# Performance work log

Measured on AMD Instinct MI355X. Metric: run time of the kernel, lower is better.

The kernel has to match this reference:

```python
import jax, jax.numpy as jnp
import numpy as np


def setup_inputs() -> dict:
    key = jax.random.key(0)
    ks = jax.random.split(key, 8)
    B, L, d_model = 2, 4096, 1024
    d_inner, d_state, d_conv, dt_rank = 2048, 16, 4, 64
    f = jnp.float32
    g = lambda k, shape, scale: jax.random.normal(k, shape, dtype=f) * scale
    # dt bias init: inverse-softplus of dt ~ U[log 1e-3, log 1e-1] (as in Mamba)
    dt = jnp.exp(jax.random.uniform(ks[5], (d_inner,), f) * (np.log(0.1) - np.log(0.001)) + np.log(0.001))
    dt = jnp.clip(dt, 1e-4, None)
    inv_dt = dt + jnp.log(-jnp.expm1(-dt))
    A_log = jnp.log(jnp.broadcast_to(jnp.arange(1, d_state + 1, dtype=f), (d_inner, d_state)))
    return {
        "hidden_states": jax.random.normal(ks[0], (B, L, d_model), f),
        "in_proj_w": g(ks[1], (2 * d_inner, d_model), 0.02),
        "conv_w": g(ks[2], (d_inner, d_conv), 0.1),
        "conv_b": jnp.zeros((d_inner,), f),
        "x_proj_w": g(ks[3], (dt_rank + 2 * d_state, d_inner), 0.02),
        "dt_proj_w": g(ks[4], (d_inner, dt_rank), dt_rank ** -0.5),
        "dt_proj_b": inv_dt,
        "A_log": A_log,
        "D": jnp.ones((d_inner,), f),
        "out_proj_w": g(ks[6], (d_model, d_inner), 0.02),
    }


def reference(hidden_states, in_proj_w, conv_w, conv_b, x_proj_w, dt_proj_w, dt_proj_b, A_log, D, out_proj_w):
    B_, L, _ = hidden_states.shape
    d_inner, d_conv = conv_w.shape
    dt_rank = dt_proj_w.shape[1]
    d_state = A_log.shape[1]

    # input projection -> x, z gates (B, L, d_inner) each
    xz = jnp.einsum('bld,ed->ble', hidden_states, in_proj_w)
    x, z = jnp.split(xz, 2, axis=-1)

    # causal depthwise conv1d over time + SiLU
    xc = jnp.transpose(x, (0, 2, 1))                       # (B, d_inner, L)
    kern = conv_w[:, None, :]                              # (O=d_inner, I/g=1, W)
    xc = jax.lax.conv_general_dilated(
        xc, kern, window_strides=(1,), padding=[(d_conv - 1, 0)],
        dimension_numbers=('NCH', 'OIH', 'NCH'), feature_group_count=d_inner)
    xc = xc + conv_b[None, :, None]
    x = jax.nn.silu(jnp.transpose(xc, (0, 2, 1)))          # (B, L, d_inner)

    # data-dependent SSM parameters
    x_dbl = jnp.einsum('bld,kd->blk', x, x_proj_w)         # (B, L, dt_rank+2n)
    dt, Bm, Cm = jnp.split(x_dbl, [dt_rank, dt_rank + d_state], axis=-1)
    dt = jnp.einsum('blr,dr->bld', dt, dt_proj_w)
    dt = jax.nn.softplus(dt + dt_proj_b)                   # delta_softplus + delta_bias
    A = -jnp.exp(A_log)                                    # (d_inner, d_state)

    # selective scan over the sequence dim; carry h: (B, d_inner, d_state)
    def step(h, inp):
        x_t, dt_t, B_t, C_t = inp                          # (B,d) (B,d) (B,n) (B,n)
        dA = jnp.exp(dt_t[..., None] * A)                  # (B, d, n)
        h = h * dA + (dt_t * x_t)[..., None] * B_t[:, None, :]
        y = jnp.einsum('bdn,bn->bd', h, C_t)
        return h, y

    h0 = jnp.zeros((B_, d_inner, d_state), x.dtype)
    xs = (jnp.transpose(x, (1, 0, 2)), jnp.transpose(dt, (1, 0, 2)),
          jnp.transpose(Bm, (1, 0, 2)), jnp.transpose(Cm, (1, 0, 2)))
    _, ys = jax.lax.scan(step, h0, xs)                     # ys: (L, B, d_inner)

    y = jnp.transpose(ys, (1, 0, 2)) + x * D               # skip via D
    y = y * jax.nn.silu(z)                                 # gate
    return jnp.einsum('bld,od->blo', y, out_proj_w)        # (B, L, d_model)
```

## Files before the change

### kernel.cpp

```cpp
#include <hip/hip_runtime.h>
#include <cmath>

#define CH 64
#define NC 64

typedef __bf16 bf16_t;
typedef __attribute__((ext_vector_type(8))) __bf16 bf16x8;
typedef __attribute__((ext_vector_type(4))) __bf16 bf16x4;
typedef __attribute__((ext_vector_type(4))) float f32x4;

#define GLOAD_LDS16(gp, lp)                                                     \
    __builtin_amdgcn_global_load_lds(                                           \
        (const __attribute__((address_space(1))) unsigned int*)(uintptr_t)(gp), \
        (__attribute__((address_space(3))) unsigned int*)(uintptr_t)(lp),       \
        16, 0, 0)

__global__ __launch_bounds__(256) void split5n(
    const float* __restrict__ a, bf16_t* __restrict__ ah, int n4a,
    const float* __restrict__ b, bf16_t* __restrict__ bh, int n4b,
    const float* __restrict__ c, bf16_t* __restrict__ ch, bf16_t* __restrict__ cl, int n4c,
    const float* __restrict__ d, bf16_t* __restrict__ dh, bf16_t* __restrict__ dl, int n4d,
    const float* __restrict__ e, bf16_t* __restrict__ eh, int n4e)
{
    int i = blockIdx.x * 256 + threadIdx.x;
    if (i < n4a) {
        const float4 v = ((const float4*)a)[i];
        bf16x4 hv = {(bf16_t)v.x, (bf16_t)v.y, (bf16_t)v.z, (bf16_t)v.w};
        ((bf16x4*)ah)[i] = hv;
        return;
    }
    i -= n4a;
    if (i < n4b) {
        const float4 v = ((const float4*)b)[i];
        bf16x4 hv = {(bf16_t)v.x, (bf16_t)v.y, (bf16_t)v.z, (bf16_t)v.w};
        ((bf16x4*)bh)[i] = hv;
        return;
    }
    i -= n4b;
    if (i >= n4c + n4d) {
        i -= n4c + n4d;
        if (i < n4e) {
            const float4 v = ((const float4*)e)[i];
            bf16x4 hv = {(bf16_t)v.x, (bf16_t)v.y, (bf16_t)v.z, (bf16_t)v.w};
            ((bf16x4*)eh)[i] = hv;
        }
        return;
    }
    const float* src; bf16_t* hp; bf16_t* lp;
    if (i < n4c) { src = c; hp = ch; lp = cl; }
    else         { i -= n4c; src = d; hp = dh; lp = dl; }

    const float4 v = ((const float4*)src)[i];
    const bf16_t h0 = (bf16_t)v.x, h1 = (bf16_t)v.y,
                 h2 = (bf16_t)v.z, h3 = (bf16_t)v.w;
    bf16x4 hv = {h0, h1, h2, h3};
    bf16x4 lv = {(bf16_t)(v.x - (float)h0), (bf16_t)(v.y - (float)h1),
                 (bf16_t)(v.z - (float)h2), (bf16_t)(v.w - (float)h3)};
    ((bf16x4*)hp)[i] = hv;
    ((bf16x4*)lp)[i] = lv;
}

__global__ __launch_bounds__(256) void add8_split(
    const float* __restrict__ p, float* __restrict__ o,
    bf16_t* __restrict__ dth, bf16_t* __restrict__ dtl,
    int n4, size_t stride4)
{
    const int i = blockIdx.x * 256 + threadIdx.x;
    if (i >= n4) return;
    float4 s = make_float4(0.f, 0.f, 0.f, 0.f);
#pragma unroll
    for (int k = 0; k < 8; ++k) {
        const float4 v = ((const float4*)p)[(size_t)k * stride4 + i];
        s.x += v.x; s.y += v.y; s.z += v.z; s.w += v.w;
    }
    ((float4*)o)[i] = s;

    const int col4 = i % 24;
    if (col4 < 16) {
        const int row = i / 24;
        const bf16_t h0 = (bf16_t)s.x, h1 = (bf16_t)s.y,
                     h2 = (bf16_t)s.z, h3 = (bf16_t)s.w;
        bf16x4 hv = {h0, h1, h2, h3};
        bf16x4 lv = {(bf16_t)(s.x - (float)h0), (bf16_t)(s.y - (float)h1),
                     (bf16_t)(s.z - (float)h2), (bf16_t)(s.w - (float)h3)};
        ((bf16x4*)dth)[(size_t)row * 16 + col4] = hv;
        ((bf16x4*)dtl)[(size_t)row * 16 + col4] = lv;
    }
}

__global__ __launch_bounds__(256) void in_proj_fused1(
    const bf16_t* __restrict__ Ah, const bf16_t* __restrict__ Wh,
    bf16_t* __restrict__ X, bf16_t* __restrict__ Z, int Ktot)
{
    __shared__ __align__(16) bf16_t Ash[128 * 32];
    __shared__ __align__(16) bf16_t Bsh[128 * 32];

    const int tid  = threadIdx.x;
    const int lane = tid & 63;
    const int w    = tid >> 6;
    const int wr   = (w >> 1) * 64;
    const int wc   = (w & 1) * 64;
    const int bm   = blockIdx.x * 128;
    const int by   = blockIdx.y;
    const int bnW  = by * 128;
    const int l16  = lane & 15;
    const int lhi  = lane >> 4;

    f32x4 acc[4][4];
#pragma unroll
    for (int i = 0; i < 4; ++i)
#pragma unroll
        for (int j = 0; j < 4; ++j)
#pragma unroll
            for (int r = 0; r < 4; ++r) acc[i][j][r] = 0.f;

    const int srow0 = tid >> 2;
    const int sks   = (tid & 3) << 3;
    const int ldsb0 = tid * 16;

    for (int k0 = 0; k0 < Ktot; k0 += 32) {
        __syncthreads();
#pragma unroll
        for (int call = 0; call < 2; ++call) {
            const int row = srow0 + call * 64;
            const int wb  = ldsb0 + call * 4096;
            GLOAD_LDS16(Ah + (size_t)(bm + row) * Ktot + k0 + sks, (char*)Ash + wb);
            GLOAD_LDS16(Wh + (size_t)(bnW + row) * Ktot + k0 + sks, (char*)Bsh + wb);
        }
        __syncthreads();

        bf16x8 af[4], bfr[4];
#pragma unroll
        for (int f = 0; f < 4; ++f) {
            af[f]  = *(const bf16x8*)&Ash[(wr + f * 16 + l16) * 32 + lhi * 8];
            bfr[f] = *(const bf16x8*)&Bsh[(wc + f * 16 + l16) * 32 + lhi * 8];
        }
#pragma unroll
        for (int fm = 0; fm < 4; ++fm)
#pragma unroll
            for (int fn = 0; fn < 4; ++fn)
                acc[fm][fn] = __builtin_amdgcn_mfma_f32_16x16x32_bf16(
                    af[fm], bfr[fn], acc[fm][fn], 0, 0, 0);
    }

    bf16_t* outp = (by < 16) ? X : Z;
    const int bnC = ((by < 16) ? by : (by - 16)) * 128;
#pragma unroll
    for (int fm = 0; fm < 4; ++fm) {
        const int row0 = bm + wr + fm * 16 + lhi * 4;
#pragma unroll
        for (int fn = 0; fn < 4; ++fn) {
            const int col = bnC + wc + fn * 16 + l16;
#pragma unroll
            for (int r = 0; r < 4; ++r)
                outp[(size_t)(row0 + r) * 2048 + col] = (bf16_t)acc[fm][fn][r];
        }
    }
}

__global__ __launch_bounds__(256) void gemm_mfma3dt(
    const bf16_t* __restrict__ Ah, const bf16_t* __restrict__ Al,
    const bf16_t* __restrict__ Bh, const bf16_t* __restrict__ Bl,
    bf16_t* __restrict__ C, const float* __restrict__ bias,
    int Ktot, int ldc)
{
    __shared__ __align__(16) bf16_t Ash[128 * 32];
    __shared__ __align__(16) bf16_t Asl[128 * 32];
    __shared__ __align__(16) bf16_t Bsh[128 * 32];
    __shared__ __align__(16) bf16_t Bsl[128 * 32];

    const int tid  = threadIdx.x;
    const int lane = tid & 63;
    const int w    = tid >> 6;
    const int wr   = (w >> 1) * 64;
    const int wc   = (w & 1) * 64;
    const int bm   = blockIdx.x * 128;
    const int bn   = blockIdx.y * 128;
    const int l16  = lane & 15;
    const int lhi  = lane >> 4;

    f32x4 acc[4][4];
#pragma unroll
    for (int i = 0; i < 4; ++i)
#pragma unroll
        for (int j = 0; j < 4; ++j)
#pragma unroll
            for (int r = 0; r < 4; ++r) acc[i][j][r] = 0.f;

    const int srow0 = tid >> 2;
    const int sks   = (tid & 3) << 3;
    const int ldsb0 = tid * 16;

    for (int k0 = 0; k0 < Ktot; k0 += 32) {
        __syncthreads();
#pragma unroll
        for (int call = 0; call < 2; ++call) {
            const int row = srow0 + call * 64;
            const int wb  = ldsb0 + call * 4096;
            const size_t aoff = (size_t)(bm + row) * Ktot + k0 + sks;
            const size_t boff = (size_t)(bn + row) * Ktot + k0 + sks;
            GLOAD_LDS16(Ah + aoff, (char*)Ash + wb);
            GLOAD_LDS16(Al + aoff, (char*)Asl + wb);
            GLOAD_LDS16(Bh + boff, (char*)Bsh + wb);
            GLOAD_LDS16(Bl + boff, (char*)Bsl + wb);
        }
        __syncthreads();

        bf16x8 ah[4], al[4], bh[4], bl[4];
#pragma unroll
        for (int f = 0; f < 4; ++f) {
            const int ar = (wr + f * 16 + l16) * 32 + lhi * 8;
            const int br = (wc + f * 16 + l16) * 32 + lhi * 8;
            ah[f] = *(const bf16x8*)&Ash[ar];
            al[f] = *(const bf16x8*)&Asl[ar];
            bh[f] = *(const bf16x8*)&Bsh[br];
            bl[f] = *(const bf16x8*)&Bsl[br];
        }
#pragma unroll
        for (int fm = 0; fm < 4; ++fm)
#pragma unroll
            for (int fn = 0; fn < 4; ++fn) {
                acc[fm][fn] = __builtin_amdgcn_mfma_f32_16x16x32_bf16(
                    ah[fm], bh[fn], acc[fm][fn], 0, 0, 0);
                acc[fm][fn] = __builtin_amdgcn_mfma_f32_16x16x32_bf16(
                    al[fm], bh[fn], acc[fm][fn], 0, 0, 0);
                acc[fm][fn] = __builtin_amdgcn_mfma_f32_16x16x32_bf16(
                    ah[fm], bl[fn], acc[fm][fn], 0, 0, 0);
            }
    }

#pragma unroll
    for (int fm = 0; fm < 4; ++fm) {
        const int row0 = bm + wr + fm * 16 + lhi * 4;
#pragma unroll
        for (int fn = 0; fn < 4; ++fn) {
            const int col = bn + wc + fn * 16 + l16;
#pragma unroll
            for (int r = 0; r < 4; ++r) {
                float v = acc[fm][fn][r] + bias[col];
                v = (v > 20.f) ? v : log1pf(expf(v));
                C[(size_t)(row0 + r) * ldc + col] = (bf16_t)v;
            }
        }
    }
}

__global__ __launch_bounds__(256) void gemm_mfma3x(
    const bf16_t* __restrict__ Ah, const bf16_t* __restrict__ Al,
    const bf16_t* __restrict__ Bh, const bf16_t* __restrict__ Bl,
    float* __restrict__ C, int Ktot, int Ksplit, size_t partStride)
{
    __shared__ __align__(16) bf16_t Ash[128 * 32];
    __shared__ __align__(16) bf16_t Asl[128 * 32];
    __shared__ __align__(16) bf16_t Bsh[128 * 32];
    __shared__ __align__(16) bf16_t Bsl[128 * 32];

    const int tid  = threadIdx.x;
    const int lane = tid & 63;
    const int w    = tid >> 6;
    const int wr   = (w >> 1) * 64;
    const int wc   = (w & 1) * 64;
    const int bm   = blockIdx.x * 128;
    const int l16  = lane & 15;
    const int lhi  = lane >> 4;

    f32x4 acc[4][4];
#pragma unroll
    for (int i = 0; i < 4; ++i)
#pragma unroll
        for (int j = 0; j < 4; ++j)
#pragma unroll
            for (int r = 0; r < 4; ++r) acc[i][j][r] = 0.f;

    const int srow0 = tid >> 2;
    const int sks   = (tid & 3) << 3;
    const int ldsb0 = tid * 16;

    const int kBeg = blockIdx.z * Ksplit;
    const int kEnd = kBeg + Ksplit;

    for (int k0 = kBeg; k0 < kEnd; k0 += 32) {
        __syncthreads();
#pragma unroll
        for (int call = 0; call < 2; ++call) {
            const int row  = srow0 + call * 64;
            const int brow = (row < 96) ? row : 95;
            const int wb   = ldsb0 + call * 4096;
            const size_t aoff = (size_t)(bm + row) * Ktot + k0 + sks;
            const size_t boff = (size_t)brow * Ktot + k0 + sks;
            GLOAD_LDS16(Ah + aoff, (char*)Ash + wb);
            GLOAD_LDS16(Al + aoff, (char*)Asl + wb);
            GLOAD_LDS16(Bh + boff, (char*)Bsh + wb);
            GLOAD_LDS16(Bl + boff, (char*)Bsl + wb);
        }
        __syncthreads();

        bf16x8 ah[4], al[4], bh[4], bl[4];
#pragma unroll
        for (int f = 0; f < 4; ++f) {
            const int ar = (wr + f * 16 + l16) * 32 + lhi * 8;
            const int br = (wc + f * 16 + l16) * 32 + lhi * 8;
            ah[f] = *(const bf16x8*)&Ash[ar];
            al[f] = *(const bf16x8*)&Asl[ar];
            bh[f] = *(const bf16x8*)&Bsh[br];
            bl[f] = *(const bf16x8*)&Bsl[br];
        }
#pragma unroll
        for (int fm = 0; fm < 4; ++fm)
#pragma unroll
            for (int fn = 0; fn < 4; ++fn) {
                acc[fm][fn] = __builtin_amdgcn_mfma_f32_16x16x32_bf16(
                    ah[fm], bh[fn], acc[fm][fn], 0, 0, 0);
                acc[fm][fn] = __builtin_amdgcn_mfma_f32_16x16x32_bf16(
                    al[fm], bh[fn], acc[fm][fn], 0, 0, 0);
                acc[fm][fn] = __builtin_amdgcn_mfma_f32_16x16x32_bf16(
                    ah[fm], bl[fn], acc[fm][fn], 0, 0, 0);
            }
    }

    float* Cp = C + (size_t)blockIdx.z * partStride;
#pragma unroll
    for (int fm = 0; fm < 4; ++fm) {
        const int row0 = bm + wr + fm * 16 + lhi * 4;
#pragma unroll
        for (int fn = 0; fn < 4; ++fn) {
            const int col = wc + fn * 16 + l16;
            if (col < 96) {
#pragma unroll
                for (int r = 0; r < 4; ++r)
                    Cp[(size_t)(row0 + r) * 96 + col] = acc[fm][fn][r];
            }
        }
    }
}

__global__ __launch_bounds__(256) void gemm_mfma1o128at(
    const bf16_t* __restrict__ Ah, const bf16_t* __restrict__ Bh,
    float* __restrict__ C, int K, int Ksplit, int ldc)
{
    __shared__ __align__(16) bf16_t Ash[128 * 32];
    __shared__ __align__(16) bf16_t Bsh[128 * 32];

    const int tid  = threadIdx.x;
    const int lane = tid & 63;
    const int w    = tid >> 6;
    const int wr   = (w >> 1) * 64;
    const int wc   = (w & 1) * 64;
    const int bm   = blockIdx.x * 128;
    const int bn   = blockIdx.y * 128;
    const int l16  = lane & 15;
    const int lhi  = lane >> 4;

    f32x4 acc[4][4];
#pragma unroll
    for (int i = 0; i < 4; ++i)
#pragma unroll
        for (int j = 0; j < 4; ++j)
#pragma unroll
            for (int r = 0; r < 4; ++r) acc[i][j][r] = 0.f;

    const int srow0 = tid >> 2;
    const int sks   = (tid & 3) << 3;
    const int ldsb0 = tid * 16;

    const int kBeg = blockIdx.z * Ksplit;
    const int kEnd = kBeg + Ksplit;

    for (int k0 = kBeg; k0 < kEnd; k0 += 32) {
        __syncthreads();
#pragma unroll
        for (int call = 0; call < 2; ++call) {
            const int row = srow0 + call * 64;
            const int wb  = ldsb0 + call * 4096;
            GLOAD_LDS16(Ah + (size_t)(bm + row) * K + k0 + sks, (char*)Ash + wb);
            GLOAD_LDS16(Bh + (size_t)(bn + row) * K + k0 + sks, (char*)Bsh + wb);
        }
        __syncthreads();

        bf16x8 af[4], bfr[4];
#pragma unroll
        for (int f = 0; f < 4; ++f) {
            af[f]  = *(const bf16x8*)&Ash[(wr + f * 16 + l16) * 32 + lhi * 8];
            bfr[f] = *(const bf16x8*)&Bsh[(wc + f * 16 + l16) * 32 + lhi * 8];
        }
#pragma unroll
        for (int fm = 0; fm < 4; ++fm)
#pragma unroll
            for (int fn = 0; fn < 4; ++fn)
                acc[fm][fn] = __builtin_amdgcn_mfma_f32_16x16x32_bf16(
                    af[fm], bfr[fn], acc[fm][fn], 0, 0, 0);
    }

#pragma unroll
    for (int fm = 0; fm < 4; ++fm) {
        const int row0 = bm + wr + fm * 16 + lhi * 4;
#pragma unroll
        for (int fn = 0; fn < 4; ++fn) {
            const int col = bn + wc + fn * 16 + l16;
#pragma unroll
            for (int r = 0; r < 4; ++r)
                atomicAdd(&C[(size_t)(row0 + r) * ldc + col], acc[fm][fn][r]);
        }
    }
}

__global__ __launch_bounds__(256) void conv_silu8b(
    const bf16_t* __restrict__ xin, const float* __restrict__ w,
    const float* __restrict__ bias,
    bf16_t* __restrict__ xh, bf16_t* __restrict__ xl,
    int L, int D)
{
    const long long e8 = (long long)blockIdx.x * 256 + threadIdx.x;
    const int Dq = D >> 3;
    const int dq = (int)(e8 % Dq);
    const long long bl = e8 / Dq;
    const int l = (int)(bl % L);
    const int d = dq << 3;
    const long long base = bl * D + d;

    float t0[8], t1[8], t2[8], t3[8];
    {
        const bf16x8 v = *(const bf16x8*)&xin[base];
#pragma unroll
        for (int j = 0; j < 8; ++j) t0[j] = (float)v[j];
    }
    if (l >= 1) { const bf16x8 v = *(const bf16x8*)&xin[base - D];
#pragma unroll
        for (int j = 0; j < 8; ++j) t1[j] = (float)v[j];
    } else { for (int j = 0; j < 8; ++j) t1[j] = 0.f; }
    if (l >= 2) { const bf16x8 v = *(const bf16x8*)&xin[base - 2 * D];
#pragma unroll
        for (int j = 0; j < 8; ++j) t2[j] = (float)v[j];
    } else { for (int j = 0; j < 8; ++j) t2[j] = 0.f; }
    if (l >= 3) { const bf16x8 v = *(const bf16x8*)&xin[base - 3 * D];
#pragma unroll
        for (int j = 0; j < 8; ++j) t3[j] = (float)v[j];
    } else { for (int j = 0; j < 8; ++j) t3[j] = 0.f; }

    bf16x8 hv, lv;
#pragma unroll
    for (int j = 0; j < 8; ++j) {
        const float4 wv = *(const float4*)&w[(d + j) * 4];
        float acc = bias[d + j];
        acc = fmaf(wv.w, t0[j], acc);
        acc = fmaf(wv.z, t1[j], acc);
        acc = fmaf(wv.y, t2[j], acc);
        acc = fmaf(wv.x, t3[j], acc);
        const float o = acc / (1.f + __expf(-acc));
        const bf16_t h = (bf16_t)o;
        hv[j] = h;
        lv[j] = (bf16_t)(o - (float)h);
    }
    *(bf16x8*)&xh[base] = hv;
    *(bf16x8*)&xl[base] = lv;
}

__global__ __launch_bounds__(256) void scan_local2(
    const bf16_t* __restrict__ xh, const bf16_t* __restrict__ xl,
    const bf16_t* __restrict__ dtb,
    const float* __restrict__ xdbl,  const float* __restrict__ A_log,
    float* __restrict__ Sbuf, float* __restrict__ Pbuf)
{
    __shared__ float Bs[CH][16];

    const int d = blockIdx.x * 256 + threadIdx.x;
    const int c = blockIdx.y;
    const int b = blockIdx.z;
    const long long rowBase = (long long)b * 4096 + (long long)c * CH;

    {
        const int e = threadIdx.x;
        const int i = e >> 2, j = (e & 3) << 2;
        *(float4*)&Bs[i][j] = *(const float4*)&xdbl[(rowBase + i) * 96 + 64 + j];
    }
    __syncthreads();

    float a[16], S[16];
#pragma unroll
    for (int n = 0; n < 16; ++n) {
        a[n] = -__expf(A_log[d * 16 + n]);
        S[n] = 0.f;
    }
    float sumdt = 0.f;

    for (int i = 0; i < CH; ++i) {
        const long long row = rowBase + i;
        const float dtv = (float)dtb[row * 2048 + d];
        const float xv  = (float)xh[row * 2048 + d] + (float)xl[row * 2048 + d];
        const float u   = dtv * xv;
        sumdt += dtv;
#pragma unroll
        for (int n = 0; n < 16; ++n) {
            const float dA = __expf(dtv * a[n]);
            S[n] = fmaf(S[n], dA, u * Bs[i][n]);
        }
    }

    const size_t base = ((((size_t)b * NC + c) * 2048) + d) * 16;
#pragma unroll
    for (int k = 0; k < 4; ++k) {
        *(float4*)&Sbuf[base + k * 4] =
            make_float4(S[k*4], S[k*4+1], S[k*4+2], S[k*4+3]);
        *(float4*)&Pbuf[base + k * 4] =
            make_float4(__expf(sumdt * a[k*4]),   __expf(sumdt * a[k*4+1]),
                        __expf(sumdt * a[k*4+2]), __expf(sumdt * a[k*4+3]));
    }
}

__global__ __launch_bounds__(256) void scan_chunk_prefix(
    float* __restrict__ Sbuf, const float* __restrict__ Pbuf)
{
    const int tid = blockIdx.x * 256 + threadIdx.x;
    const int b  = tid >> 15;
    const int dn = tid & 32767;

    float H = 0.f;
    for (int c = 0; c < NC; ++c) {
        const size_t idx = ((size_t)b * NC + c) * 32768 + dn;
        const float S = Sbuf[idx];
        const float P = Pbuf[idx];
        Sbuf[idx] = H;
        H = fmaf(P, H, S);
    }
}

__global__ __launch_bounds__(256) void scan_final2(
    const bf16_t* __restrict__ xh, const bf16_t* __restrict__ xl,
    const bf16_t* __restrict__ dtb,
    const float* __restrict__ xdbl,  const float* __restrict__ A_log,
    const float* __restrict__ Dp,    const bf16_t* __restrict__ z,
    const float* __restrict__ Hbuf,  bf16_t* __restrict__ y)
{
    __shared__ float BCs[CH][32];

    const int d = blockIdx.x * 256 + threadIdx.x;
    const int c = blockIdx.y;
    const int b = blockIdx.z;
    const long long rowBase = (long long)b * 4096 + (long long)c * CH;

#pragma unroll
    for (int k = 0; k < 2; ++k) {
        const int e = k * 256 + threadIdx.x;
        const int i = e >> 3, j = (e & 7) << 2;
        *(float4*)&BCs[i][j] = *(const float4*)&xdbl[(rowBase + i) * 96 + 64 + j];
    }
    __syncthreads();

    float a[16], h[16];
    const size_t hbase = ((((size_t)b * NC + c) * 2048) + d) * 16;
#pragma unroll
    for (int k = 0; k < 4; ++k) {
        const float4 hv = *(const float4*)&Hbuf[hbase + k * 4];
        h[k*4] = hv.x; h[k*4+1] = hv.y; h[k*4+2] = hv.z; h[k*4+3] = hv.w;
    }
#pragma unroll
    for (int n = 0; n < 16; ++n) a[n] = -__expf(A_log[d * 16 + n]);
    const float Dv = Dp[d];

    for (int i = 0; i < CH; ++i) {
        const long long row = rowBase + i;
        const float dtv = (float)dtb[row * 2048 + d];
        const float xv  = (float)xh[row * 2048 + d] + (float)xl[row * 2048 + d];
        const float u   = dtv * xv;
        float acc = 0.f;
#pragma unroll
        for (int n = 0; n < 16; ++n) {
            const float dA = __expf(dtv * a[n]);
            h[n] = fmaf(h[n], dA, u * BCs[i][n]);
            acc  = fmaf(h[n], BCs[i][16 + n], acc);
        }
        const float zv = (float)z[row * 2048 + d];
        float yv = acc + xv * Dv;
        yv = yv * (zv / (1.f + __expf(-zv)));
        y[row * 2048 + d] = (bf16_t)yv;
    }
}

extern "C" void kernel_launch(void* const* d_in, const int* in_sizes, int n_in,
                              void* d_out, int out_size, void* d_ws, size_t ws_size,
                              hipStream_t stream)
{
    const float* hidden     = (const float*)d_in[0];
    const float* in_proj_w  = (const float*)d_in[1];
    const float* conv_w     = (const float*)d_in[2];
    const float* conv_b     = (const float*)d_in[3];
    const float* x_proj_w   = (const float*)d_in[4];
    const float* dt_proj_w  = (const float*)d_in[5];
    const float* dt_proj_b  = (const float*)d_in[6];
    const float* A_log      = (const float*)d_in[7];
    const float* Dvec       = (const float*)d_in[8];
    const float* out_proj_w = (const float*)d_in[9];
    float* out = (float*)d_out;

    const int L = 4096, dinner = 2048, dmodel = 1024;
    const int M = 2 * L;

    float* z     = (float*)d_ws;
    float* xraw  = z     + (size_t)M * dinner;
    float* xconv = xraw  + (size_t)M * dinner;
    float* xdbl  = xconv + (size_t)M * dinner;
    float* Sbuf  = xdbl  + (size_t)M * 96;

    bf16_t* w1_h  = (bf16_t*)Sbuf;
    bf16_t* hid_h = (bf16_t*)xconv;
    bf16_t* zb    = (bf16_t*)z;
    bf16_t* Xb    = (bf16_t*)xraw;
    bf16_t* xc_h  = (bf16_t*)xconv;
    bf16_t* xc_l  = xc_h + (size_t)M * dinner;
    float*  xp_part = xraw;
    bf16_t* dtb  = (bf16_t*)xraw;
    bf16_t* dth  = (bf16_t*)Sbuf;
    bf16_t* dtl  = dth + (size_t)M * 64;
    bf16_t* wdh  = (bf16_t*)out;
    bf16_t* wdl  = wdh + (size_t)dinner * 64;
    bf16_t* xpwh = (bf16_t*)xdbl;
    bf16_t* xpwl = xpwh + (size_t)96 * dinner;
    bf16_t* w2_h = zb + (size_t)M * dinner;
    float*  Pbuf = (float*)(w2_h + (size_t)dmodel * dinner);

    const int n4a = M * dmodel / 4;
    const int n4b = 2 * dinner * dmodel / 4;
    const int n4c = dinner * 64 / 4;
    const int n4d = 96 * dinner / 4;
    const int n4e = dmodel * dinner / 4;
    split5n<<<(n4a + n4b + n4c + n4d + n4e + 255) / 256, 256, 0, stream>>>(
        hidden, hid_h, n4a,
        in_proj_w, w1_h, n4b,
        dt_proj_w, wdh, wdl, n4c,
        x_proj_w, xpwh, xpwl, n4d,
        out_proj_w, w2_h, n4e);

    in_proj_fused1<<<dim3(M / 128, 32), 256, 0, stream>>>(
        hid_h, w1_h, Xb, zb, dmodel);

    conv_silu8b<<<(M * (long long)dinner / 8) / 256, 256, 0, stream>>>(
        Xb, conv_w, conv_b, xc_h, xc_l, L, dinner);

    gemm_mfma3x<<<dim3(M / 128, 1, 8), 256, 0, stream>>>(
        xc_h, xc_l, xpwh, xpwl, xp_part, dinner, dinner / 8, (size_t)M * 96);
    add8_split<<<(M * 96 / 4 + 255) / 256, 256, 0, stream>>>(
        xp_part, xdbl, dth, dtl, M * 96 / 4, (size_t)M * 96 / 4);

    gemm_mfma3dt<<<dim3(M / 128, 2048 / 128), 256, 0, stream>>>(
        dth, dtl, wdh, wdl, dtb, dt_proj_b, 64, 2048);

    scan_local2<<<dim3(dinner / 256, NC, 2), 256, 0, stream>>>(
        xc_h, xc_l, dtb, xdbl, A_log, Sbuf, Pbuf);
    scan_chunk_prefix<<<256, 256, 0, stream>>>(Sbuf, Pbuf);
    scan_final2<<<dim3(dinner / 256, NC, 2), 256, 0, stream>>>(
        xc_h, xc_l, dtb, xdbl, A_log, Dvec, zb, Sbuf, xc_h);

    hipMemsetAsync(out, 0, (size_t)M * dmodel * sizeof(float), stream);
    gemm_mfma1o128at<<<dim3(M / 128, 1024 / 128, 2), 256, 0, stream>>>(
        xc_h, w2_h, out, dinner, dinner / 2, 1024);
}
```

Baseline: 480.1 us.

## Drop low-order bf16 split of conv output and remove split-K atomics in out_proj

Stores the post-conv activations as a single bf16 array instead of a hi/lo pair. This removes the low-part write in the conv kernel, one load and one MFMA per fragment pair in the x_proj GEMM, and the extra loads in both scan kernels. The output projection drops its two-way split-K with atomicAdd and the preceding memset, writing results directly with a full-K loop per tile. The cost is lower precision on the SSM input activations and half as many blocks in the final GEMM.

```diff
diff --git a/kernel.cpp b/kernel.cpp
--- a/kernel.cpp
+++ b/kernel.cpp
@@ -245,13 +245,12 @@
     }
 }
 
-__global__ __launch_bounds__(256) void gemm_mfma3x(
-    const bf16_t* __restrict__ Ah, const bf16_t* __restrict__ Al,
+__global__ __launch_bounds__(256) void gemm_mfma2x(
+    const bf16_t* __restrict__ Ah,
     const bf16_t* __restrict__ Bh, const bf16_t* __restrict__ Bl,
     float* __restrict__ C, int Ktot, int Ksplit, size_t partStride)
 {
     __shared__ __align__(16) bf16_t Ash[128 * 32];
-    __shared__ __align__(16) bf16_t Asl[128 * 32];
     __shared__ __align__(16) bf16_t Bsh[128 * 32];
     __shared__ __align__(16) bf16_t Bsl[128 * 32];
 
@@ -289,19 +288,17 @@
             const size_t aoff = (size_t)(bm + row) * Ktot + k0 + sks;
             const size_t boff = (size_t)brow * Ktot + k0 + sks;
             GLOAD_LDS16(Ah + aoff, (char*)Ash + wb);
-            GLOAD_LDS16(Al + aoff, (char*)Asl + wb);
             GLOAD_LDS16(Bh + boff, (char*)Bsh + wb);
             GLOAD_LDS16(Bl + boff, (char*)Bsl + wb);
         }
         __syncthreads();
 
-        bf16x8 ah[4], al[4], bh[4], bl[4];
+        bf16x8 ah[4], bh[4], bl[4];
 #pragma unroll
         for (int f = 0; f < 4; ++f) {
             const int ar = (wr + f * 16 + l16) * 32 + lhi * 8;
             const int br = (wc + f * 16 + l16) * 32 + lhi * 8;
             ah[f] = *(const bf16x8*)&Ash[ar];
-            al[f] = *(const bf16x8*)&Asl[ar];
             bh[f] = *(const bf16x8*)&Bsh[br];
             bl[f] = *(const bf16x8*)&Bsl[br];
         }
@@ -312,8 +309,6 @@
                 acc[fm][fn] = __builtin_amdgcn_mfma_f32_16x16x32_bf16(
                     ah[fm], bh[fn], acc[fm][fn], 0, 0, 0);
                 acc[fm][fn] = __builtin_amdgcn_mfma_f32_16x16x32_bf16(
-                    al[fm], bh[fn], acc[fm][fn], 0, 0, 0);
-                acc[fm][fn] = __builtin_amdgcn_mfma_f32_16x16x32_bf16(
                     ah[fm], bl[fn], acc[fm][fn], 0, 0, 0);
             }
     }
@@ -334,9 +329,9 @@
     }
 }
 
-__global__ __launch_bounds__(256) void gemm_mfma1o128at(
+__global__ __launch_bounds__(256) void gemm_mfma1o128(
     const bf16_t* __restrict__ Ah, const bf16_t* __restrict__ Bh,
-    float* __restrict__ C, int K, int Ksplit, int ldc)
+    float* __restrict__ C, int K, int ldc)
 {
     __shared__ __align__(16) bf16_t Ash[128 * 32];
     __shared__ __align__(16) bf16_t Bsh[128 * 32];
@@ -363,10 +358,7 @@
     const int sks   = (tid & 3) << 3;
     const int ldsb0 = tid * 16;
 
-    const int kBeg = blockIdx.z * Ksplit;
-    const int kEnd = kBeg + Ksplit;
-
-    for (int k0 = kBeg; k0 < kEnd; k0 += 32) {
+    for (int k0 = 0; k0 < K; k0 += 32) {
         __syncthreads();
 #pragma unroll
         for (int call = 0; call < 2; ++call) {
@@ -399,15 +391,15 @@
             const int col = bn + wc + fn * 16 + l16;
 #pragma unroll
             for (int r = 0; r < 4; ++r)
-                atomicAdd(&C[(size_t)(row0 + r) * ldc + col], acc[fm][fn][r]);
-        }
-    }
-}
-
-__global__ __launch_bounds__(256) void conv_silu8b(
+                C[(size_t)(row0 + r) * ldc + col] = acc[fm][fn][r];
+        }
+    }
+}
+
+__global__ __launch_bounds__(256) void conv_silu8s(
     const bf16_t* __restrict__ xin, const float* __restrict__ w,
     const float* __restrict__ bias,
-    bf16_t* __restrict__ xh, bf16_t* __restrict__ xl,
+    bf16_t* __restrict__ xh,
     int L, int D)
 {
     const long long e8 = (long long)blockIdx.x * 256 + threadIdx.x;
@@ -437,7 +429,7 @@
         for (int j = 0; j < 8; ++j) t3[j] = (float)v[j];
     } else { for (int j = 0; j < 8; ++j) t3[j] = 0.f; }
 
-    bf16x8 hv, lv;
+    bf16x8 hv;
 #pragma unroll
     for (int j = 0; j < 8; ++j) {
         const float4 wv = *(const float4*)&w[(d + j) * 4];
@@ -447,16 +439,13 @@
         acc = fmaf(wv.y, t2[j], acc);
         acc = fmaf(wv.x, t3[j], acc);
         const float o = acc / (1.f + __expf(-acc));
-        const bf16_t h = (bf16_t)o;
-        hv[j] = h;
-        lv[j] = (bf16_t)(o - (float)h);
+        hv[j] = (bf16_t)o;
     }
     *(bf16x8*)&xh[base] = hv;
-    *(bf16x8*)&xl[base] = lv;
 }
 
 __global__ __launch_bounds__(256) void scan_local2(
-    const bf16_t* __restrict__ xh, const bf16_t* __restrict__ xl,
+    const bf16_t* __restrict__ xh,
     const bf16_t* __restrict__ dtb,
     const float* __restrict__ xdbl,  const float* __restrict__ A_log,
     float* __restrict__ Sbuf, float* __restrict__ Pbuf)
@@ -486,7 +475,7 @@
     for (int i = 0; i < CH; ++i) {
         const long long row = rowBase + i;
         const float dtv = (float)dtb[row * 2048 + d];
-        const float xv  = (float)xh[row * 2048 + d] + (float)xl[row * 2048 + d];
+        const float xv  = (float)xh[row * 2048 + d];
         const float u   = dtv * xv;
         sumdt += dtv;
 #pragma unroll
@@ -525,7 +514,7 @@
 }
 
 __global__ __launch_bounds__(256) void scan_final2(
-    const bf16_t* __restrict__ xh, const bf16_t* __restrict__ xl,
+    const bf16_t* __restrict__ xh,
     const bf16_t* __restrict__ dtb,
     const float* __restrict__ xdbl,  const float* __restrict__ A_log,
     const float* __restrict__ Dp,    const bf16_t* __restrict__ z,
@@ -560,7 +549,7 @@
     for (int i = 0; i < CH; ++i) {
         const long long row = rowBase + i;
         const float dtv = (float)dtb[row * 2048 + d];
-        const float xv  = (float)xh[row * 2048 + d] + (float)xl[row * 2048 + d];
+        const float xv  = (float)xh[row * 2048 + d];
         const float u   = dtv * xv;
         float acc = 0.f;
 #pragma unroll
@@ -606,7 +595,6 @@
     bf16_t* zb    = (bf16_t*)z;
     bf16_t* Xb    = (bf16_t*)xraw;
     bf16_t* xc_h  = (bf16_t*)xconv;
-    bf16_t* xc_l  = xc_h + (size_t)M * dinner;
     float*  xp_part = xraw;
     bf16_t* dtb  = (bf16_t*)xraw;
     bf16_t* dth  = (bf16_t*)Sbuf;
@@ -633,11 +621,11 @@
     in_proj_fused1<<<dim3(M / 128, 32), 256, 0, stream>>>(
         hid_h, w1_h, Xb, zb, dmodel);
 
-    conv_silu8b<<<(M * (long long)dinner / 8) / 256, 256, 0, stream>>>(
-        Xb, conv_w, conv_b, xc_h, xc_l, L, dinner);
-
-    gemm_mfma3x<<<dim3(M / 128, 1, 8), 256, 0, stream>>>(
-        xc_h, xc_l, xpwh, xpwl, xp_part, dinner, dinner / 8, (size_t)M * 96);
+    conv_silu8s<<<(M * (long long)dinner / 8) / 256, 256, 0, stream>>>(
+        Xb, conv_w, conv_b, xc_h, L, dinner);
+
+    gemm_mfma2x<<<dim3(M / 128, 1, 8), 256, 0, stream>>>(
+        xc_h, xpwh, xpwl, xp_part, dinner, dinner / 8, (size_t)M * 96);
     add8_split<<<(M * 96 / 4 + 255) / 256, 256, 0, stream>>>(
         xp_part, xdbl, dth, dtl, M * 96 / 4, (size_t)M * 96 / 4);
 
@@ -645,12 +633,11 @@
         dth, dtl, wdh, wdl, dtb, dt_proj_b, 64, 2048);
 
     scan_local2<<<dim3(dinner / 256, NC, 2), 256, 0, stream>>>(
-        xc_h, xc_l, dtb, xdbl, A_log, Sbuf, Pbuf);
+        xc_h, dtb, xdbl, A_log, Sbuf, Pbuf);
     scan_chunk_prefix<<<256, 256, 0, stream>>>(Sbuf, Pbuf);
     scan_final2<<<dim3(dinner / 256, NC, 2), 256, 0, stream>>>(
-        xc_h, xc_l, dtb, xdbl, A_log, Dvec, zb, Sbuf, xc_h);
-
-    hipMemsetAsync(out, 0, (size_t)M * dmodel * sizeof(float), stream);
-    gemm_mfma1o128at<<<dim3(M / 128, 1024 / 128, 2), 256, 0, stream>>>(
-        xc_h, w2_h, out, dinner, dinner / 2, 1024);
-}
+        xc_h, dtb, xdbl, A_log, Dvec, zb, Sbuf, xc_h);
+
+    gemm_mfma1o128<<<dim3(M / 128, 1024 / 128), 256, 0, stream>>>(
+        xc_h, w2_h, out, dinner, 1024);
+}
```

After: 439.3 us. 8.5% less time.
